# Kernel tuning notes

Measured on AMD Instinct MI355X. Metric: run time of the kernel, lower is better.

The kernel has to match this reference:

```python
import jax, jax.numpy as jnp
import numpy as np
from itertools import combinations, product

NQ = 10
DIM = 2 ** NQ
DEPTH = 1
ENC_PAIRS = [(q, q + 1) for q in range(0, NQ - 1, 2)] + [(q, q + 1) for q in range(1, NQ - 1, 2)]  # brick layer: even then odd
PYR = [(i, i + 1) for layer in range(NQ - 1) for i in range(NQ - layer - 1)]  # pyramid RBS wire pairs (45)
OBS_PAIRS = list(combinations(range(NQ), 2))  # 45 pairwise 2-local observables

_P = {'I': np.eye(2, dtype=np.complex128),
      'X': np.array([[0, 1], [1, 0]], dtype=np.complex128),
      'Y': np.array([[0, -1j], [1j, 0]], dtype=np.complex128),
      'Z': np.array([[1, 0], [0, -1]], dtype=np.complex128)}
_WORDS = [''.join(w) for w in product('IXYZ', repeat=2)][1:]  # PennyLane pauli_basis order, identity excluded
P15 = jnp.asarray(np.stack([np.kron(_P[w[0]], _P[w[1]]) for w in _WORDS]).astype(np.complex64))
XXm = jnp.asarray(np.kron(_P['X'], _P['X']).astype(np.complex64))
YYm = jnp.asarray(np.kron(_P['Y'], _P['Y']).astype(np.complex64))
ZZm = jnp.asarray(np.kron(_P['Z'], _P['Z']).astype(np.complex64))
I4 = jnp.eye(4, dtype=jnp.complex64)
_TRIL_I, _TRIL_J = np.tril_indices(4, -1)  # order matches create_Hermitian's count+j indexing


def _u3(t, p, l):
    c = jnp.cos(t / 2).astype(jnp.complex64)
    s = jnp.sin(t / 2).astype(jnp.complex64)
    return jnp.stack([jnp.stack([c, -jnp.exp(1j * l) * s]),
                      jnp.stack([jnp.exp(1j * p) * s, jnp.exp(1j * (p + l)) * c])])


def _ising(phi, P):
    # exp(-i*phi/2 * P) for P in {XX, YY, ZZ} (P^2 = I)
    return jnp.cos(phi / 2) * I4 - 1j * jnp.sin(phi / 2) * P


def _apply1(psi, U, w):
    # psi: (B, 2, ..., 2); single-qubit gate U (2,2) on wire w
    psi = jnp.moveaxis(psi, 1 + w, -1)
    sh = psi.shape
    out = jnp.einsum('ij,brj->bri', U, psi.reshape(sh[0], -1, 2)).reshape(sh)
    return jnp.moveaxis(out, -1, 1 + w)


def _apply2(psi, U, a, b):
    # two-qubit gate on wires (a,b), a is most-significant (PennyLane wire order). U: (4,4) or batched (B,4,4)
    psi = jnp.moveaxis(psi, (1 + a, 1 + b), (-2, -1))
    sh = psi.shape
    flat = psi.reshape(sh[0], -1, 4)
    eq = 'bij,brj->bri' if U.ndim == 3 else 'ij,brj->bri'
    out = jnp.einsum(eq, U, flat).reshape(sh)
    return jnp.moveaxis(out, (-2, -1), (1 + a, 1 + b))


def _build_H(A, B, D):
    # create_Hermitian: lower triangle A+iB, diag[0:3] = D[1:4], diag[3]=0, then h + h^dagger
    n = A.shape[0]
    h = jnp.zeros((n, 4, 4), jnp.complex64)
    h = h.at[:, _TRIL_I, _TRIL_J].set(A.astype(jnp.complex64) + 1j * B.astype(jnp.complex64))
    d = np.arange(3)
    h = h.at[:, d, d].set(D[:, 1:4].astype(jnp.complex64))
    return h + jnp.conj(jnp.swapaxes(h, -1, -2))


def setup_inputs() -> dict:
    key = jax.random.key(0)
    ks = jax.random.split(key, 9)
    f32 = jnp.float32
    return {
        'x': jax.random.normal(ks[0], (256, 512), f32),
        'W1': jax.random.normal(ks[1], (512, 256), f32) * (512 ** -0.5),
        'b1': jnp.zeros((256,), f32),
        'W2': jax.random.normal(ks[2], (256, 135), f32) * (256 ** -0.5),
        'b2': jnp.zeros((135,), f32),
        'qvit_params': 0.01 * jax.random.normal(ks[3], (DEPTH, len(PYR), 12), f32),
        'A': 2.0 * jax.random.normal(ks[4], (len(OBS_PAIRS), 6), f32),
        'B': 2.0 * jax.random.normal(ks[5], (len(OBS_PAIRS), 6), f32),
        'D': 2.0 * jax.random.normal(ks[6], (len(OBS_PAIRS), 4), f32),
    }


def reference(x, W1, b1, W2, b2, qvit_params, A, B, D):
    Bsz = x.shape[0]
    # enc_proj: Linear -> SiLU -> Linear
    enc = jax.nn.silu(x @ W1 + b1) @ W2 + b2  # (B, 135)
    # Brick-layer SpecialUnitary encoding: U = exp(i * sum theta_m P_m) via eigh
    theta = enc.reshape(Bsz, len(ENC_PAIRS), 15).astype(jnp.complex64)
    Hg = jnp.einsum('bgm,mij->bgij', theta, P15)  # Hermitian generators (B, 9, 4, 4)
    ew, V = jnp.linalg.eigh(Hg)
    Ue = jnp.einsum('bgik,bgk,bgjk->bgij', V, jnp.exp(1j * ew.astype(jnp.complex64)), jnp.conj(V))
    # |0...0>
    psi = jnp.zeros((Bsz, DIM), jnp.complex64).at[:, 0].set(1.0).reshape((Bsz,) + (2,) * NQ)
    for g, (a, b) in enumerate(ENC_PAIRS):
        psi = _apply2(psi, Ue[:, g], a, b)
    # QViT pyramid ansatz
    for ly in range(DEPTH):
        for g, (a, b) in enumerate(PYR):
            p = qvit_params[ly, g]
            psi = _apply1(psi, _u3(p[0], p[1], p[2]), a)
            psi = _apply2(psi, _ising(p[3], XXm), a, b)
            psi = _apply2(psi, _ising(p[4], YYm), a, b)
            psi = _apply2(psi, _ising(p[5], ZZm), a, b)
            psi = _apply1(psi, _u3(p[6], p[7], p[8]), a)
            psi = _apply2(psi, _ising(p[9], XXm), a, b)
            psi = _apply2(psi, _ising(p[10], YYm), a, b)
            psi = _apply2(psi, _ising(p[11], ZZm), a, b)
    # Pairwise ANO Hermitian expectations
    Hobs = _build_H(A, B, D)  # (45, 4, 4)
    outs = []
    for w, (a, b) in enumerate(OBS_PAIRS):
        pm = jnp.moveaxis(psi, (1 + a, 1 + b), (1, 2)).reshape(Bsz, 4, -1)
        outs.append(jnp.real(jnp.einsum('bir,ij,bjr->b', jnp.conj(pm), Hobs[w], pm)))
    return jnp.stack(outs, axis=1).astype(jnp.float32)
```

## Files before the change

### kernel.cpp

```cpp
#include <hip/hip_runtime.h>
#include <math.h>

#define NOBS 45
typedef float2 c32;

constexpr int W2Sc[10] = {1, 0, 7, 6, 5, 3, 2, 4, 9, 8};
constexpr int OAc[NOBS] = {
    0,0,0,0,0,0,0,0,0, 1,1,1,1,1,1,1,1, 2,2,2,2,2,2,2, 3,3,3,3,3,3,
    4,4,4,4,4, 5,5,5,5, 6,6,6, 7,7, 8};
constexpr int OBc[NOBS] = {
    1,2,3,4,5,6,7,8,9, 2,3,4,5,6,7,8,9, 3,4,5,6,7,8,9, 4,5,6,7,8,9,
    5,6,7,8,9, 6,7,8,9, 7,8,9, 8,9, 9};
constexpr int TIc[6] = {1, 2, 2, 3, 3, 3};
constexpr int TJc[6] = {0, 0, 1, 0, 1, 2};

__device__ __forceinline__ c32 cfma(c32 a, c32 b, c32 c) {
    c.x = fmaf(a.x, b.x, fmaf(-a.y, b.y, c.x));
    c.y = fmaf(a.x, b.y, fmaf(a.y, b.x, c.y));
    return c;
}
__device__ __forceinline__ c32 cmul(c32 a, c32 b) {
    return make_float2(a.x * b.x - a.y * b.y, a.x * b.y + a.y * b.x);
}

template <int CTRL>
__device__ __forceinline__ float dppf(float x) {
    return __uint_as_float((unsigned)__builtin_amdgcn_update_dpp(
        0, (int)__float_as_uint(x), CTRL, 0xF, 0xF, true));
}
__device__ __forceinline__ float swap32f(float a) {
    auto r = __builtin_amdgcn_permlane32_swap(__float_as_uint(a), __float_as_uint(a), false, false);
    return (__uint_as_float(r[0]) + __uint_as_float(r[1])) - a;
}
#if __has_builtin(__builtin_amdgcn_permlane16_swap)
__device__ __forceinline__ float swap16f(float a) {
    auto r = __builtin_amdgcn_permlane16_swap(__float_as_uint(a), __float_as_uint(a), false, false);
    return (__uint_as_float(r[0]) + __uint_as_float(r[1])) - a;
}
#else
__device__ __forceinline__ float swap16f(float a) { return __shfl_xor(a, 16, 64); }
#endif
__device__ __forceinline__ float swz4f(float a) {
    return __uint_as_float(__builtin_amdgcn_ds_swizzle(__float_as_uint(a), 0x101F));
}
template <int M>
__device__ __forceinline__ float exf(float x) {
    float r = x;
    if constexpr ((M & 3) == 1) r = dppf<0xB1>(r);
    else if constexpr ((M & 3) == 2) r = dppf<0x4E>(r);
    else if constexpr ((M & 3) == 3) r = dppf<0x1B>(r);
    if constexpr (M & 4)  r = swz4f(r);
    if constexpr (M & 8)  r = dppf<0x128>(r);
    if constexpr (M & 16) r = swap16f(r);
    if constexpr (M & 32) r = swap32f(r);
    return r;
}
template <int M>
__device__ __forceinline__ c32 exch(c32 a) { return make_float2(exf<M>(a.x), exf<M>(a.y)); }
__device__ __forceinline__ c32 swap32c(c32 a) { return make_float2(swap32f(a.x), swap32f(a.y)); }

__device__ __forceinline__ float wave_reduce63(float x) {
    x += dppf<0x111>(x);
    x += dppf<0x112>(x);
    x += dppf<0x114>(x);
    x += dppf<0x118>(x);
    x += dppf<0x142>(x);
    x += dppf<0x143>(x);
    return x;
}

__device__ __forceinline__ int insert2(int t, int pl, int ph) {
    int low  = t & ((1 << pl) - 1);
    int rest = t >> pl;
    int nm   = ph - 1 - pl;
    int mid  = rest & ((1 << nm) - 1);
    int high = rest >> nm;
    return low | (mid << (pl + 1)) | (high << (ph + 1));
}

template <int W>
__device__ __forceinline__ c32 pE(int r, int c) {
    if constexpr (W == 0) return make_float2((r == c) ? 1.f : 0.f, 0.f);
    else if constexpr (W == 1) return make_float2((r != c) ? 1.f : 0.f, 0.f);
    else if constexpr (W == 2) return make_float2(0.f, (r == c) ? 0.f : ((r == 0) ? -1.f : 1.f));
    else return make_float2((r == c) ? ((r == 0) ? 1.f : -1.f) : 0.f, 0.f);
}
template <int W0, int W1>
__device__ __forceinline__ void paccum(c32& H, float th, int i1, int i2, int j1, int j2) {
    c32 a = pE<W0>(i1, j1), b = pE<W1>(i2, j2);
    c32 p = cmul(a, b);
    H.x = fmaf(th, p.x, H.x);
    H.y = fmaf(th, p.y, H.y);
}

__device__ __forceinline__ void gate_LL(c32 v[4], const c32* __restrict__ U) {
    c32 n0 = cfma(U[0],  v[0], cfma(U[1],  v[1], cfma(U[2],  v[2], cmul(U[3],  v[3]))));
    c32 n1 = cfma(U[4],  v[0], cfma(U[5],  v[1], cfma(U[6],  v[2], cmul(U[7],  v[3]))));
    c32 n2 = cfma(U[8],  v[0], cfma(U[9],  v[1], cfma(U[10], v[2], cmul(U[11], v[3]))));
    c32 n3 = cfma(U[12], v[0], cfma(U[13], v[1], cfma(U[14], v[2], cmul(U[15], v[3]))));
    v[0] = n0; v[1] = n1; v[2] = n2; v[3] = n3;
}

__device__ __forceinline__ void gate_LocLane5(c32 v[4], const c32* __restrict__ U, int ln) {
    int bb = (ln >> 5) & 1;
    c32 p0 = swap32c(v[0]), p1 = swap32c(v[1]), p2 = swap32c(v[2]), p3 = swap32c(v[3]);
    int c00 = bb, c01 = 2 | bb, c10 = bb ^ 1, c11 = 2 | (bb ^ 1);
    const c32* U0 = U + bb * 4;
    const c32* U1 = U + (2 | bb) * 4;
    {
        c32 n0 = cfma(U0[c00], v[0], cfma(U0[c01], v[1], cfma(U0[c10], p0, cmul(U0[c11], p1))));
        c32 n1 = cfma(U1[c00], v[0], cfma(U1[c01], v[1], cfma(U1[c10], p0, cmul(U1[c11], p1))));
        v[0] = n0; v[1] = n1;
    }
    {
        c32 n2 = cfma(U0[c00], v[2], cfma(U0[c01], v[3], cfma(U0[c10], p2, cmul(U0[c11], p3))));
        c32 n3 = cfma(U1[c00], v[2], cfma(U1[c01], v[3], cfma(U1[c10], p2, cmul(U1[c11], p3))));
        v[2] = n2; v[3] = n3;
    }
}

template <int QA, int QB>
__device__ __forceinline__ void gate_LaneLane(c32 v[4], const c32* __restrict__ U, int ln) {
    int bA = (ln >> QA) & 1, bB = (ln >> QB) & 1;
    int r = (bA << 1) | bB;
    const c32* Ur = U + r * 4;
    c32 uS = Ur[r], uB = Ur[r ^ 1], uA = Ur[r ^ 2], uC = Ur[r ^ 3];
#pragma unroll
    for (int lc = 0; lc < 4; lc++) {
        c32 pB = exch<(1 << QB)>(v[lc]);
        c32 pA = exch<(1 << QA)>(v[lc]);
        c32 pC = exch<(1 << QA)>(pB);
        v[lc] = cfma(uS, v[lc], cfma(uB, pB, cfma(uA, pA, cmul(uC, pC))));
    }
}

template <int PA, int PB>
__device__ __forceinline__ void lds_apply(const c32* __restrict__ U, c32* psi, int tid) {
    const int PL = (PA < PB) ? PA : PB, PH = (PA < PB) ? PB : PA;
    int base = insert2(tid, PL, PH);
    const int oa = 1 << PA, ob = 1 << PB;
    c32 g0 = psi[base], g1 = psi[base + ob], g2 = psi[base + oa], g3 = psi[base + oa + ob];
    c32 n0 = cfma(U[0],  g0, cfma(U[1],  g1, cfma(U[2],  g2, cmul(U[3],  g3))));
    c32 n1 = cfma(U[4],  g0, cfma(U[5],  g1, cfma(U[6],  g2, cmul(U[7],  g3))));
    c32 n2 = cfma(U[8],  g0, cfma(U[9],  g1, cfma(U[10], g2, cmul(U[11], g3))));
    c32 n3 = cfma(U[12], g0, cfma(U[13], g1, cfma(U[14], g2, cmul(U[15], g3))));
    psi[base] = n0; psi[base + ob] = n1; psi[base + oa] = n2; psi[base + oa + ob] = n3;
}
template <int PA, int PB>
__device__ __forceinline__ void gate_LDS(c32 v[4], const c32* __restrict__ U, c32* psi, int tid) {
#pragma unroll
    for (int lc = 0; lc < 4; lc++) psi[(tid << 2) | lc] = v[lc];
    __syncthreads();
    lds_apply<PA, PB>(U, psi, tid);
    __syncthreads();
#pragma unroll
    for (int lc = 0; lc < 4; lc++) v[lc] = psi[(tid << 2) | lc];
}
template <int PA1, int PB1, int PA2, int PB2>
__device__ __forceinline__ void gate_LDS2(c32 v[4], const c32* __restrict__ U1,
                                          const c32* __restrict__ U2, c32* psi, int tid) {
#pragma unroll
    for (int lc = 0; lc < 4; lc++) psi[(tid << 2) | lc] = v[lc];
    __syncthreads();
    lds_apply<PA1, PB1>(U1, psi, tid);
    __syncthreads();
    lds_apply<PA2, PB2>(U2, psi, tid);
    __syncthreads();
#pragma unroll
    for (int lc = 0; lc < 4; lc++) v[lc] = psi[(tid << 2) | lc];
}

__global__ __launch_bounds__(256, 1) void mega_kernel(
    const float* __restrict__ x,  const float* __restrict__ W1, const float* __restrict__ b1,
    const float* __restrict__ W2, const float* __restrict__ b2, const float* __restrict__ qp,
    const float* __restrict__ Am, const float* __restrict__ Bm, const float* __restrict__ Dm,
    float* __restrict__ out) {
    __shared__ c32 psiS[1024];
    __shared__ c32 UeS[144];
    __shared__ c32 GpS[720];
    __shared__ float HbS[720];
    __shared__ float encS[136];
    __shared__ float redS[180];

    const int b = blockIdx.x, t = threadIdx.x, ln = t & 63;
    float* F = (float*)psiS;

    if (t < 128) ((float4*)F)[t] = ((const float4*)(x + (size_t)b * 512))[t];
    __syncthreads();
    {
        int q = t & 63, sl = t >> 6;
        float4 a4 = make_float4(0.f, 0.f, 0.f, 0.f);
#pragma unroll 16
        for (int kk = 0; kk < 128; kk++) {
            int k = sl * 128 + kk;
            float xk = F[k];
            const float4 w = *(const float4*)(W1 + (size_t)k * 256 + q * 4);
            a4.x = fmaf(xk, w.x, a4.x); a4.y = fmaf(xk, w.y, a4.y);
            a4.z = fmaf(xk, w.z, a4.z); a4.w = fmaf(xk, w.w, a4.w);
        }
        *(float4*)(F + 512 + sl * 256 + q * 4) = a4;
    }
    __syncthreads();
    {
        float hv = b1[t] + F[512 + t] + F[768 + t] + F[1024 + t] + F[1280 + t];
        hv = hv / (1.f + __expf(-hv));
        F[1536 + t] = hv;
    }
    __syncthreads();
    if (t < 135) {
        float a2 = b2[t], a3 = 0.f;
#pragma unroll 16
        for (int k = 0; k < 128; k++) {
            a2 = fmaf(F[1536 + k],       W2[(size_t)k * 135 + t],         a2);
            a3 = fmaf(F[1536 + 128 + k], W2[(size_t)(128 + k) * 135 + t], a3);
        }
        encS[t] = a2 + a3;
    }
    __syncthreads();

    c32* Mm = psiS;
    c32* Rb = psiS + 144;
    c32* TA = psiS + 288;
    if (t < 144) {
        int m = t >> 4, e = t & 15, i = e >> 2, j = e & 3;
        int i1 = i >> 1, i2 = i & 1, j1 = j >> 1, j2 = j & 1;
        const float* th = encS + m * 15;
        c32 H = make_float2(0.f, 0.f);
        paccum<0,1>(H, th[0],  i1,i2,j1,j2); paccum<0,2>(H, th[1],  i1,i2,j1,j2);
        paccum<0,3>(H, th[2],  i1,i2,j1,j2); paccum<1,0>(H, th[3],  i1,i2,j1,j2);
        paccum<1,1>(H, th[4],  i1,i2,j1,j2); paccum<1,2>(H, th[5],  i1,i2,j1,j2);
        paccum<1,3>(H, th[6],  i1,i2,j1,j2); paccum<2,0>(H, th[7],  i1,i2,j1,j2);
        paccum<2,1>(H, th[8],  i1,i2,j1,j2); paccum<2,2>(H, th[9],  i1,i2,j1,j2);
        paccum<2,3>(H, th[10], i1,i2,j1,j2); paccum<3,0>(H, th[11], i1,i2,j1,j2);
        paccum<3,1>(H, th[12], i1,i2,j1,j2); paccum<3,2>(H, th[13], i1,i2,j1,j2);
        paccum<3,3>(H, th[14], i1,i2,j1,j2);
        const float sc = 1.f / 64.f;
        Mm[t] = make_float2(-H.y * sc, H.x * sc);
        Rb[t] = make_float2((i == j) ? 1.f : 0.f, 0.f);
    } else if (t >= 234) {
        for (int w = t - 234; w < NOBS; w += 22) {
            float* Hf = HbS + w * 16;
            Hf[0] = 2.f * Dm[w * 4 + 1];
            Hf[1] = 2.f * Dm[w * 4 + 2];
            Hf[2] = 2.f * Dm[w * 4 + 3];
            Hf[3] = 0.f;
#pragma unroll
            for (int k = 0; k < 6; k++) {
                Hf[4 + 2 * k] = 2.f * Am[w * 6 + k];
                Hf[5 + 2 * k] = 2.f * Bm[w * 6 + k];
            }
        }
    }
    __syncthreads();
    c32 Mrow[4];
    if (t < 144) {
        int m = t >> 4, i = (t & 15) >> 2;
#pragma unroll
        for (int k = 0; k < 4; k++) Mrow[k] = Mm[m * 16 + i * 4 + k];
    }
    for (int step = 0; step < 13; step++) {
        if (t < 144) {
            int m = t >> 4, e = t & 15, i = e >> 2, j = e & 3;
            const c32* cur = (step & 1) ? UeS : Rb;
            c32 acc = make_float2(0.f, 0.f);
            c32 outv;
            if (step < 7) {
#pragma unroll
                for (int k = 0; k < 4; k++) acc = cfma(Mrow[k], cur[m * 16 + k * 4 + j], acc);
                float inv = 1.f / (float)(7 - step);
                outv = make_float2(fmaf(acc.x, inv, (i == j) ? 1.f : 0.f), acc.y * inv);
            } else {
#pragma unroll
                for (int k = 0; k < 4; k++)
                    acc = cfma(cur[m * 16 + i * 4 + k], cur[m * 16 + k * 4 + j], acc);
                outv = acc;
            }
            ((step & 1) ? Rb : UeS)[t] = outv;
        } else if (t >= 144 && t < 234 && step < 8) {
            int pt = t - 144, g = pt >> 1, ih = (pt & 1) << 1;
            const float* p = qp + g * 12;
            const c32* src = ((step & 1) ? TA : GpS) + g * 16;
            c32* dst = ((step & 1) ? GpS : TA) + g * 16;
#pragma unroll
            for (int r2 = 0; r2 < 2; r2++) {
                int i = ih + r2, i1 = i >> 1, i2 = i & 1;
                c32 row[4];
                if (step == 0) {
                    float s, c; __sincosf(p[0] * 0.5f, &s, &c);
                    c32 u0, u1;
                    if (i1 == 0) { u0 = make_float2(c, 0.f);
                                   u1 = make_float2(-__cosf(p[2]) * s, -__sinf(p[2]) * s); }
                    else { u0 = make_float2(__cosf(p[1]) * s, __sinf(p[1]) * s);
                           u1 = make_float2(__cosf(p[1] + p[2]) * c, __sinf(p[1] + p[2]) * c); }
#pragma unroll
                    for (int jj = 0; jj < 4; jj++) row[jj] = make_float2(0.f, 0.f);
                    row[i2] = u0; row[2 | i2] = u1;
                } else {
                    c32 coef0, coef1; int c0, c1;
                    if (step == 1 || step == 5) {
                        float s, c; __sincosf(p[step == 1 ? 3 : 9] * 0.5f, &s, &c);
                        c0 = i; coef0 = make_float2(c, 0.f);
                        c1 = i ^ 3; coef1 = make_float2(0.f, -s);
                    } else if (step == 2 || step == 6) {
                        float s, c; __sincosf(p[step == 2 ? 4 : 10] * 0.5f, &s, &c);
                        float yy = (i == 0 || i == 3) ? 1.f : -1.f;
                        c0 = i; coef0 = make_float2(c, 0.f);
                        c1 = i ^ 3; coef1 = make_float2(0.f, s * yy);
                    } else if (step == 3 || step == 7) {
                        float s, c; __sincosf(p[step == 3 ? 5 : 11] * 0.5f, &s, &c);
                        float zz = (i == 0 || i == 3) ? 1.f : -1.f;
                        c0 = i; coef0 = make_float2(c, -s * zz);
                        c1 = i; coef1 = make_float2(0.f, 0.f);
                    } else {
                        float s, c; __sincosf(p[6] * 0.5f, &s, &c);
                        if (i1 == 0) { coef0 = make_float2(c, 0.f);
                                       coef1 = make_float2(-__cosf(p[8]) * s, -__sinf(p[8]) * s); }
                        else { coef0 = make_float2(__cosf(p[7]) * s, __sinf(p[7]) * s);
                               coef1 = make_float2(__cosf(p[7] + p[8]) * c, __sinf(p[7] + p[8]) * c); }
                        c0 = i2; c1 = 2 | i2;
                    }
#pragma unroll
                    for (int jj = 0; jj < 4; jj++)
                        row[jj] = cfma(coef0, src[c0 * 4 + jj], cmul(coef1, src[c1 * 4 + jj]));
                }
#pragma unroll
                for (int jj = 0; jj < 4; jj++) dst[i * 4 + jj] = row[jj];
            }
        }
        __syncthreads();
    }

    c32 v[4];
#pragma unroll
    for (int lc = 0; lc < 4; lc++) v[lc] = make_float2(0.f, 0.f);
    if (t == 0) v[0] = make_float2(1.f, 0.f);

    gate_LL(v, UeS + 0);
    gate_LaneLane<5, 4>(v, UeS + 16, ln);
    gate_LaneLane<3, 1>(v, UeS + 32, ln);
    gate_LaneLane<0, 2>(v, UeS + 48, ln);
    gate_LDS<9, 8>(v, UeS + 64, psiS, t);
    gate_LocLane5(v, UeS + 80, ln);
    gate_LaneLane<4, 3>(v, UeS + 96, ln);
    gate_LaneLane<1, 0>(v, UeS + 112, ln);
    gate_LDS<4, 9>(v, UeS + 128, psiS, t);

    {
        int g = 0;
#pragma unroll
        for (int layer = 0; layer < 9; layer++) {
            int amax = 8 - layer;
            gate_LL(v, GpS + (g++) * 16);
            if (amax >= 1) gate_LocLane5(v, GpS + (g++) * 16, ln);
            if (amax >= 2) gate_LaneLane<5, 4>(v, GpS + (g++) * 16, ln);
            if (amax >= 3) gate_LaneLane<4, 3>(v, GpS + (g++) * 16, ln);
            if (amax >= 4) gate_LaneLane<3, 1>(v, GpS + (g++) * 16, ln);
            if (amax >= 5) gate_LaneLane<1, 0>(v, GpS + (g++) * 16, ln);
            if (amax >= 6) gate_LaneLane<0, 2>(v, GpS + (g++) * 16, ln);
            if (amax >= 8) { gate_LDS2<4, 9, 9, 8>(v, GpS + g * 16, GpS + (g + 1) * 16, psiS, t); g += 2; }
            else if (amax >= 7) gate_LDS<4, 9>(v, GpS + (g++) * 16, psiS, t);
        }
    }

#pragma unroll
    for (int lc = 0; lc < 4; lc++) psiS[(t << 2) | lc] = v[lc];
    __syncthreads();
#pragma unroll
    for (int w0 = 0; w0 < NOBS; w0 += 5) {
        float pr[5];
#pragma unroll
        for (int u = 0; u < 5; u++) {
            const int w = w0 + u;
            const int pa = W2Sc[OAc[w]], pb = W2Sc[OBc[w]];
            const int pl = (pa < pb) ? pa : pb, phh = (pa < pb) ? pb : pa;
            int base = insert2(t, pl, phh);
            const int oa = 1 << pa, ob = 1 << pb;
            c32 vg[4];
            vg[0] = psiS[base];      vg[1] = psiS[base + ob];
            vg[2] = psiS[base + oa]; vg[3] = psiS[base + oa + ob];
            const float* Hf = HbS + w * 16;
            float r = Hf[0] * fmaf(vg[0].x, vg[0].x, vg[0].y * vg[0].y)
                    + Hf[1] * fmaf(vg[1].x, vg[1].x, vg[1].y * vg[1].y)
                    + Hf[2] * fmaf(vg[2].x, vg[2].x, vg[2].y * vg[2].y);
#pragma unroll
            for (int k = 0; k < 6; k++) {
                c32 vi = vg[TIc[k]], vj = vg[TJc[k]];
                float cx = fmaf(vi.x, vj.x, vi.y * vj.y);
                float cy = fmaf(vi.x, vj.y, -vi.y * vj.x);
                r = fmaf(Hf[4 + 2 * k], cx, r);
                r = fmaf(-Hf[5 + 2 * k], cy, r);
            }
            pr[u] = wave_reduce63(r);
        }
        if (ln == 63) {
#pragma unroll
            for (int u = 0; u < 5; u++) redS[(w0 + u) * 4 + (t >> 6)] = pr[u];
        }
    }
    __syncthreads();
    if (t < NOBS)
        out[(size_t)b * NOBS + t] = redS[t * 4] + redS[t * 4 + 1] + redS[t * 4 + 2] + redS[t * 4 + 3];
}

extern "C" void kernel_launch(void* const* d_in, const int* in_sizes, int n_in,
                              void* d_out, int out_size, void* d_ws, size_t ws_size,
                              hipStream_t stream) {
    (void)in_sizes; (void)n_in; (void)out_size; (void)d_ws; (void)ws_size;
    const float* x  = (const float*)d_in[0];
    const float* W1 = (const float*)d_in[1];
    const float* b1 = (const float*)d_in[2];
    const float* W2 = (const float*)d_in[3];
    const float* b2 = (const float*)d_in[4];
    const float* qp = (const float*)d_in[5];
    const float* Am = (const float*)d_in[6];
    const float* Bm = (const float*)d_in[7];
    const float* Dm = (const float*)d_in[8];
    float* out = (float*)d_out;

    hipLaunchKernelGGL(mega_kernel, dim3(256), dim3(256), 0, stream,
                       x, W1, b1, W2, b2, qp, Am, Bm, Dm, out);
}
```

Before: 107.6 us.

## Pad LDS state layout per-register plane and hoist gate coefficient loads

Stores the state vector in LDS as four padded planes (stride 257) indexed by register slot instead of interleaved tid*4+lc, so that dump/reload and the gather accesses in LDS gates and observables hit fewer bank conflicts. Gate matrix coefficients for each layer are now loaded from shared memory into registers up front, before the chain of lane-exchange gate applications, so the loads are issued early and their latency overlaps the math. This raises register pressure and makes the LDS index arithmetic more complex.

After: 107.2 us. Within noise of the previous version (-0.3%).

```diff
diff --git a/kernel.cpp b/kernel.cpp
--- a/kernel.cpp
+++ b/kernel.cpp
@@ -13,6 +13,8 @@
     5,6,7,8,9, 6,7,8,9, 7,8,9, 8,9, 9};
 constexpr int TIc[6] = {1, 2, 2, 3, 3, 3};
 constexpr int TJc[6] = {0, 0, 1, 0, 1, 2};
+
+#define PSTRIDE 257
 
 __device__ __forceinline__ c32 cfma(c32 a, c32 b, c32 c) {
     c.x = fmaf(a.x, b.x, fmaf(-a.y, b.y, c.x));
@@ -93,81 +95,83 @@
     H.y = fmaf(th, p.y, H.y);
 }
 
-__device__ __forceinline__ void gate_LL(c32 v[4], const c32* __restrict__ U) {
-    c32 n0 = cfma(U[0],  v[0], cfma(U[1],  v[1], cfma(U[2],  v[2], cmul(U[3],  v[3]))));
-    c32 n1 = cfma(U[4],  v[0], cfma(U[5],  v[1], cfma(U[6],  v[2], cmul(U[7],  v[3]))));
-    c32 n2 = cfma(U[8],  v[0], cfma(U[9],  v[1], cfma(U[10], v[2], cmul(U[11], v[3]))));
-    c32 n3 = cfma(U[12], v[0], cfma(U[13], v[1], cfma(U[14], v[2], cmul(U[15], v[3]))));
-    v[0] = n0; v[1] = n1; v[2] = n2; v[3] = n3;
-}
-
-__device__ __forceinline__ void gate_LocLane5(c32 v[4], const c32* __restrict__ U, int ln) {
+struct F16 { c32 u[16]; };
+struct FLoc { c32 a[4]; c32 b[4]; };
+struct F4 { c32 uS, uB, uA, uC; };
+
+__device__ __forceinline__ F16 loadF16(const c32* __restrict__ U) {
+    F16 f;
+#pragma unroll
+    for (int i = 0; i < 16; i++) f.u[i] = U[i];
+    return f;
+}
+__device__ __forceinline__ FLoc loadLoc(const c32* __restrict__ U, int ln) {
     int bb = (ln >> 5) & 1;
-    c32 p0 = swap32c(v[0]), p1 = swap32c(v[1]), p2 = swap32c(v[2]), p3 = swap32c(v[3]);
-    int c00 = bb, c01 = 2 | bb, c10 = bb ^ 1, c11 = 2 | (bb ^ 1);
     const c32* U0 = U + bb * 4;
     const c32* U1 = U + (2 | bb) * 4;
-    {
-        c32 n0 = cfma(U0[c00], v[0], cfma(U0[c01], v[1], cfma(U0[c10], p0, cmul(U0[c11], p1))));
-        c32 n1 = cfma(U1[c00], v[0], cfma(U1[c01], v[1], cfma(U1[c10], p0, cmul(U1[c11], p1))));
-        v[0] = n0; v[1] = n1;
-    }
-    {
-        c32 n2 = cfma(U0[c00], v[2], cfma(U0[c01], v[3], cfma(U0[c10], p2, cmul(U0[c11], p3))));
-        c32 n3 = cfma(U1[c00], v[2], cfma(U1[c01], v[3], cfma(U1[c10], p2, cmul(U1[c11], p3))));
-        v[2] = n2; v[3] = n3;
-    }
-}
-
+    int c00 = bb, c01 = 2 | bb, c10 = bb ^ 1, c11 = 2 | (bb ^ 1);
+    FLoc f;
+    f.a[0] = U0[c00]; f.a[1] = U0[c01]; f.a[2] = U0[c10]; f.a[3] = U0[c11];
+    f.b[0] = U1[c00]; f.b[1] = U1[c01]; f.b[2] = U1[c10]; f.b[3] = U1[c11];
+    return f;
+}
 template <int QA, int QB>
-__device__ __forceinline__ void gate_LaneLane(c32 v[4], const c32* __restrict__ U, int ln) {
+__device__ __forceinline__ F4 loadL2(const c32* __restrict__ U, int ln) {
     int bA = (ln >> QA) & 1, bB = (ln >> QB) & 1;
     int r = (bA << 1) | bB;
     const c32* Ur = U + r * 4;
-    c32 uS = Ur[r], uB = Ur[r ^ 1], uA = Ur[r ^ 2], uC = Ur[r ^ 3];
+    F4 f;
+    f.uS = Ur[r]; f.uB = Ur[r ^ 1]; f.uA = Ur[r ^ 2]; f.uC = Ur[r ^ 3];
+    return f;
+}
+
+__device__ __forceinline__ void applyLL(c32 v[4], const F16& f) {
+    c32 n0 = cfma(f.u[0],  v[0], cfma(f.u[1],  v[1], cfma(f.u[2],  v[2], cmul(f.u[3],  v[3]))));
+    c32 n1 = cfma(f.u[4],  v[0], cfma(f.u[5],  v[1], cfma(f.u[6],  v[2], cmul(f.u[7],  v[3]))));
+    c32 n2 = cfma(f.u[8],  v[0], cfma(f.u[9],  v[1], cfma(f.u[10], v[2], cmul(f.u[11], v[3]))));
+    c32 n3 = cfma(f.u[12], v[0], cfma(f.u[13], v[1], cfma(f.u[14], v[2], cmul(f.u[15], v[3]))));
+    v[0] = n0; v[1] = n1; v[2] = n2; v[3] = n3;
+}
+__device__ __forceinline__ void applyLoc(c32 v[4], const FLoc& f) {
+    c32 p0 = swap32c(v[0]), p1 = swap32c(v[1]), p2 = swap32c(v[2]), p3 = swap32c(v[3]);
+    c32 n0 = cfma(f.a[0], v[0], cfma(f.a[1], v[1], cfma(f.a[2], p0, cmul(f.a[3], p1))));
+    c32 n1 = cfma(f.b[0], v[0], cfma(f.b[1], v[1], cfma(f.b[2], p0, cmul(f.b[3], p1))));
+    c32 n2 = cfma(f.a[0], v[2], cfma(f.a[1], v[3], cfma(f.a[2], p2, cmul(f.a[3], p3))));
+    c32 n3 = cfma(f.b[0], v[2], cfma(f.b[1], v[3], cfma(f.b[2], p2, cmul(f.b[3], p3))));
+    v[0] = n0; v[1] = n1; v[2] = n2; v[3] = n3;
+}
+template <int QA, int QB>
+__device__ __forceinline__ void applyL2(c32 v[4], const F4& f) {
 #pragma unroll
     for (int lc = 0; lc < 4; lc++) {
         c32 pB = exch<(1 << QB)>(v[lc]);
         c32 pA = exch<(1 << QA)>(v[lc]);
         c32 pC = exch<(1 << QA)>(pB);
-        v[lc] = cfma(uS, v[lc], cfma(uB, pB, cfma(uA, pA, cmul(uC, pC))));
-    }
-}
-
+        v[lc] = cfma(f.uS, v[lc], cfma(f.uB, pB, cfma(f.uA, pA, cmul(f.uC, pC))));
+    }
+}
+
+__device__ __forceinline__ void dumpV(const c32 v[4], c32* __restrict__ psiR, int t) {
+#pragma unroll
+    for (int lc = 0; lc < 4; lc++) psiR[lc * PSTRIDE + t] = v[lc];
+}
+__device__ __forceinline__ void loadV(c32 v[4], const c32* __restrict__ psiR, int t) {
+#pragma unroll
+    for (int lc = 0; lc < 4; lc++) v[lc] = psiR[lc * PSTRIDE + t];
+}
 template <int PA, int PB>
-__device__ __forceinline__ void lds_apply(const c32* __restrict__ U, c32* psi, int tid) {
-    const int PL = (PA < PB) ? PA : PB, PH = (PA < PB) ? PB : PA;
-    int base = insert2(tid, PL, PH);
-    const int oa = 1 << PA, ob = 1 << PB;
-    c32 g0 = psi[base], g1 = psi[base + ob], g2 = psi[base + oa], g3 = psi[base + oa + ob];
-    c32 n0 = cfma(U[0],  g0, cfma(U[1],  g1, cfma(U[2],  g2, cmul(U[3],  g3))));
-    c32 n1 = cfma(U[4],  g0, cfma(U[5],  g1, cfma(U[6],  g2, cmul(U[7],  g3))));
-    c32 n2 = cfma(U[8],  g0, cfma(U[9],  g1, cfma(U[10], g2, cmul(U[11], g3))));
-    c32 n3 = cfma(U[12], g0, cfma(U[13], g1, cfma(U[14], g2, cmul(U[15], g3))));
-    psi[base] = n0; psi[base + ob] = n1; psi[base + oa] = n2; psi[base + oa + ob] = n3;
-}
-template <int PA, int PB>
-__device__ __forceinline__ void gate_LDS(c32 v[4], const c32* __restrict__ U, c32* psi, int tid) {
-#pragma unroll
-    for (int lc = 0; lc < 4; lc++) psi[(tid << 2) | lc] = v[lc];
-    __syncthreads();
-    lds_apply<PA, PB>(U, psi, tid);
-    __syncthreads();
-#pragma unroll
-    for (int lc = 0; lc < 4; lc++) v[lc] = psi[(tid << 2) | lc];
-}
-template <int PA1, int PB1, int PA2, int PB2>
-__device__ __forceinline__ void gate_LDS2(c32 v[4], const c32* __restrict__ U1,
-                                          const c32* __restrict__ U2, c32* psi, int tid) {
-#pragma unroll
-    for (int lc = 0; lc < 4; lc++) psi[(tid << 2) | lc] = v[lc];
-    __syncthreads();
-    lds_apply<PA1, PB1>(U1, psi, tid);
-    __syncthreads();
-    lds_apply<PA2, PB2>(U2, psi, tid);
-    __syncthreads();
-#pragma unroll
-    for (int lc = 0; lc < 4; lc++) v[lc] = psi[(tid << 2) | lc];
+__device__ __forceinline__ void ldsApply(const F16& f, c32* __restrict__ psiR, int t) {
+    constexpr int PL = (PA < PB) ? PA : PB, PH = (PA < PB) ? PB : PA;
+    int base = insert2(t, PL, PH);
+    c32* pl_ = psiR + (base & 3) * PSTRIDE;
+    int s = base >> 2;
+    constexpr int oa = (1 << PA) >> 2, ob = (1 << PB) >> 2;
+    c32 g0 = pl_[s], g1 = pl_[s + ob], g2 = pl_[s + oa], g3 = pl_[s + oa + ob];
+    c32 n0 = cfma(f.u[0],  g0, cfma(f.u[1],  g1, cfma(f.u[2],  g2, cmul(f.u[3],  g3))));
+    c32 n1 = cfma(f.u[4],  g0, cfma(f.u[5],  g1, cfma(f.u[6],  g2, cmul(f.u[7],  g3))));
+    c32 n2 = cfma(f.u[8],  g0, cfma(f.u[9],  g1, cfma(f.u[10], g2, cmul(f.u[11], g3))));
+    c32 n3 = cfma(f.u[12], g0, cfma(f.u[13], g1, cfma(f.u[14], g2, cmul(f.u[15], g3))));
+    pl_[s] = n0; pl_[s + ob] = n1; pl_[s + oa] = n2; pl_[s + oa + ob] = n3;
 }
 
 __global__ __launch_bounds__(256, 1) void mega_kernel(
@@ -175,7 +179,7 @@
     const float* __restrict__ W2, const float* __restrict__ b2, const float* __restrict__ qp,
     const float* __restrict__ Am, const float* __restrict__ Bm, const float* __restrict__ Dm,
     float* __restrict__ out) {
-    __shared__ c32 psiS[1024];
+    __shared__ __align__(16) c32 psiRaw[4 * PSTRIDE];
     __shared__ c32 UeS[144];
     __shared__ c32 GpS[720];
     __shared__ float HbS[720];
@@ -183,7 +187,7 @@
     __shared__ float redS[180];
 
     const int b = blockIdx.x, t = threadIdx.x, ln = t & 63;
-    float* F = (float*)psiS;
+    float* F = (float*)psiRaw;
 
     if (t < 128) ((float4*)F)[t] = ((const float4*)(x + (size_t)b * 512))[t];
     __syncthreads();
@@ -218,9 +222,9 @@
     }
     __syncthreads();
 
-    c32* Mm = psiS;
-    c32* Rb = psiS + 144;
-    c32* TA = psiS + 288;
+    c32* Mm = psiRaw;
+    c32* Rb = psiRaw + 144;
+    c32* TA = psiRaw + 288;
     if (t < 144) {
         int m = t >> 4, e = t & 15, i = e >> 2, j = e & 3;
         int i1 = i >> 1, i2 = i & 1, j1 = j >> 1, j2 = j & 1;
@@ -335,35 +339,72 @@
     for (int lc = 0; lc < 4; lc++) v[lc] = make_float2(0.f, 0.f);
     if (t == 0) v[0] = make_float2(1.f, 0.f);
 
-    gate_LL(v, UeS + 0);
-    gate_LaneLane<5, 4>(v, UeS + 16, ln);
-    gate_LaneLane<3, 1>(v, UeS + 32, ln);
-    gate_LaneLane<0, 2>(v, UeS + 48, ln);
-    gate_LDS<9, 8>(v, UeS + 64, psiS, t);
-    gate_LocLane5(v, UeS + 80, ln);
-    gate_LaneLane<4, 3>(v, UeS + 96, ln);
-    gate_LaneLane<1, 0>(v, UeS + 112, ln);
-    gate_LDS<4, 9>(v, UeS + 128, psiS, t);
+    {
+        F16 e0 = loadF16(UeS + 0);
+        F4 e1 = loadL2<5, 4>(UeS + 16, ln);
+        F4 e2 = loadL2<3, 1>(UeS + 32, ln);
+        F4 e3 = loadL2<0, 2>(UeS + 48, ln);
+        applyLL(v, e0);
+        applyL2<5, 4>(v, e1);
+        applyL2<3, 1>(v, e2);
+        applyL2<0, 2>(v, e3);
+        F16 e4 = loadF16(UeS + 64);
+        dumpV(v, psiRaw, t); __syncthreads();
+        ldsApply<9, 8>(e4, psiRaw, t); __syncthreads();
+        loadV(v, psiRaw, t);
+        FLoc e5 = loadLoc(UeS + 80, ln);
+        F4 e6 = loadL2<4, 3>(UeS + 96, ln);
+        F4 e7 = loadL2<1, 0>(UeS + 112, ln);
+        applyLoc(v, e5);
+        applyL2<4, 3>(v, e6);
+        applyL2<1, 0>(v, e7);
+        F16 e8 = loadF16(UeS + 128);
+        dumpV(v, psiRaw, t); __syncthreads();
+        ldsApply<4, 9>(e8, psiRaw, t); __syncthreads();
+        loadV(v, psiRaw, t);
+    }
 
     {
         int g = 0;
 #pragma unroll
         for (int layer = 0; layer < 9; layer++) {
-            int amax = 8 - layer;
-            gate_LL(v, GpS + (g++) * 16);
-            if (amax >= 1) gate_LocLane5(v, GpS + (g++) * 16, ln);
-            if (amax >= 2) gate_LaneLane<5, 4>(v, GpS + (g++) * 16, ln);
-            if (amax >= 3) gate_LaneLane<4, 3>(v, GpS + (g++) * 16, ln);
-            if (amax >= 4) gate_LaneLane<3, 1>(v, GpS + (g++) * 16, ln);
-            if (amax >= 5) gate_LaneLane<1, 0>(v, GpS + (g++) * 16, ln);
-            if (amax >= 6) gate_LaneLane<0, 2>(v, GpS + (g++) * 16, ln);
-            if (amax >= 8) { gate_LDS2<4, 9, 9, 8>(v, GpS + g * 16, GpS + (g + 1) * 16, psiS, t); g += 2; }
-            else if (amax >= 7) gate_LDS<4, 9>(v, GpS + (g++) * 16, psiS, t);
-        }
-    }
-
-#pragma unroll
-    for (int lc = 0; lc < 4; lc++) psiS[(t << 2) | lc] = v[lc];
+            const int amax = 8 - layer;
+            F16 f0 = loadF16(GpS + g * 16);
+            FLoc f1; F4 f2, f3, f4, f5, f6;
+            int gi = g + 1;
+            if (amax >= 1) f1 = loadLoc(GpS + (gi++) * 16, ln);
+            if (amax >= 2) f2 = loadL2<5, 4>(GpS + (gi++) * 16, ln);
+            if (amax >= 3) f3 = loadL2<4, 3>(GpS + (gi++) * 16, ln);
+            if (amax >= 4) f4 = loadL2<3, 1>(GpS + (gi++) * 16, ln);
+            if (amax >= 5) f5 = loadL2<1, 0>(GpS + (gi++) * 16, ln);
+            if (amax >= 6) f6 = loadL2<0, 2>(GpS + (gi++) * 16, ln);
+            applyLL(v, f0);
+            if (amax >= 1) applyLoc(v, f1);
+            if (amax >= 2) applyL2<5, 4>(v, f2);
+            if (amax >= 3) applyL2<4, 3>(v, f3);
+            if (amax >= 4) applyL2<3, 1>(v, f4);
+            if (amax >= 5) applyL2<1, 0>(v, f5);
+            if (amax >= 6) applyL2<0, 2>(v, f6);
+            g = gi;
+            if (amax >= 8) {
+                F16 h1 = loadF16(GpS + g * 16);
+                F16 h2 = loadF16(GpS + (g + 1) * 16);
+                dumpV(v, psiRaw, t); __syncthreads();
+                ldsApply<4, 9>(h1, psiRaw, t); __syncthreads();
+                ldsApply<9, 8>(h2, psiRaw, t); __syncthreads();
+                loadV(v, psiRaw, t);
+                g += 2;
+            } else if (amax >= 7) {
+                F16 h1 = loadF16(GpS + g * 16);
+                dumpV(v, psiRaw, t); __syncthreads();
+                ldsApply<4, 9>(h1, psiRaw, t); __syncthreads();
+                loadV(v, psiRaw, t);
+                g += 1;
+            }
+        }
+    }
+
+    dumpV(v, psiRaw, t);
     __syncthreads();
 #pragma unroll
     for (int w0 = 0; w0 < NOBS; w0 += 5) {
@@ -373,11 +414,14 @@
             const int w = w0 + u;
             const int pa = W2Sc[OAc[w]], pb = W2Sc[OBc[w]];
             const int pl = (pa < pb) ? pa : pb, phh = (pa < pb) ? pb : pa;
-            int base = insert2(t, pl, phh);
             const int oa = 1 << pa, ob = 1 << pb;
+            int i0 = insert2(t, pl, phh);
+            int i1 = i0 + ob, i2 = i0 + oa, i3 = i0 + oa + ob;
             c32 vg[4];
-            vg[0] = psiS[base];      vg[1] = psiS[base + ob];
-            vg[2] = psiS[base + oa]; vg[3] = psiS[base + oa + ob];
+            vg[0] = psiRaw[(i0 & 3) * PSTRIDE + (i0 >> 2)];
+            vg[1] = psiRaw[(i1 & 3) * PSTRIDE + (i1 >> 2)];
+            vg[2] = psiRaw[(i2 & 3) * PSTRIDE + (i2 >> 2)];
+            vg[3] = psiRaw[(i3 & 3) * PSTRIDE + (i3 >> 2)];
             const float* Hf = HbS + w * 16;
             float r = Hf[0] * fmaf(vg[0].x, vg[0].x, vg[0].y * vg[0].y)
                     + Hf[1] * fmaf(vg[1].x, vg[1].x, vg[1].y * vg[1].y)
```
